# Optimization experiments

Hardware: AMD Instinct MI355X
Metric: run time of the kernel (lower is better)

Reference implementation:

```python
import jax, jax.numpy as jnp
import numpy as np

B, S, D = 2, 2048, 2048
H, KVH, HD = 16, 4, 128
ROT = 64  # partial rotary dims (cos/sin last dim = ROT//2)
WINDOW = 1024
EPS = 1e-6


def _rmsnorm(x, scale=None):
    x32 = x.astype(jnp.float32)
    y = x32 * jax.lax.rsqrt(jnp.mean(x32 * x32, axis=-1, keepdims=True) + EPS)
    if scale is not None:
        y = y * (1.0 + scale.astype(jnp.float32))
    return y.astype(x.dtype)


def _rope(x, cos, sin):
    # x: [b, h, s, hd]; rotate first ROT dims, pass through the rest
    x_rot, x_pass = x[..., :ROT], x[..., ROT:]
    x1, x2 = x_rot[..., :ROT // 2], x_rot[..., ROT // 2:]
    rotated = jnp.concatenate([-x2, x1], axis=-1)
    cos_f = jnp.concatenate([cos, cos], axis=-1)[None, None].astype(x.dtype)
    sin_f = jnp.concatenate([sin, sin], axis=-1)[None, None].astype(x.dtype)
    return jnp.concatenate([x_rot * cos_f + rotated * sin_f, x_pass], axis=-1)


def setup_inputs() -> dict:
    key = jax.random.key(0)
    ks = jax.random.split(key, 6)
    x = jax.random.normal(ks[0], (B, S, D), jnp.float32)
    # causal + sliding-window mask (True = masked out)
    i = jnp.arange(S)
    rel = i[:, None] - i[None, :]  # query - key
    mask = (rel < 0) | (rel >= WINDOW)
    # RoPE tables
    inv_freq = 1.0 / (10000.0 ** (jnp.arange(0, ROT, 2, dtype=jnp.float32) / ROT))
    t = jnp.arange(S, dtype=jnp.float32)[:, None] * inv_freq[None, :]  # [S, ROT//2]
    cos, sin = jnp.cos(t), jnp.sin(t)
    init = 0.02
    Wq = jax.random.normal(ks[1], (D, H * HD), jnp.float32) * init
    Wk = jax.random.normal(ks[2], (D, KVH * HD), jnp.float32) * init
    Wv = jax.random.normal(ks[3], (D, KVH * HD), jnp.float32) * init
    Wo = jax.random.normal(ks[4], (H * HD, D), jnp.float32) * init
    q_scale = jnp.zeros((HD,), jnp.float32)  # Gemma RMSNorm weight init = 0, applied as (1+w)
    k_scale = jnp.zeros((HD,), jnp.float32)
    return {"x": x, "mask": mask, "cos": cos, "sin": sin,
            "Wq": Wq, "Wk": Wk, "Wv": Wv, "Wo": Wo,
            "q_scale": q_scale, "k_scale": k_scale}


def reference(x, mask, cos, sin, Wq, Wk, Wv, Wo, q_scale, k_scale):
    b, s, _ = x.shape
    G = H // KVH  # group size
    q = (x @ Wq).reshape(b, s, H, HD).transpose(0, 2, 1, 3)      # [b,H,s,hd]
    q = _rope(_rmsnorm(q, q_scale), cos, sin)
    k = (x @ Wk).reshape(b, s, KVH, HD).transpose(0, 2, 1, 3)    # [b,KVH,s,hd]
    k = _rope(_rmsnorm(k, k_scale), cos, sin)
    v = _rmsnorm((x @ Wv).reshape(b, s, KVH, HD).transpose(0, 2, 1, 3))
    # grouped-head attention (equivalent to repeat_interleave of k/v over groups)
    qg = q.reshape(b, KVH, G, s, HD)
    scores = jnp.einsum('bkgqd,bkld->bkgql', qg, k)              # no 1/sqrt(hd): QK-norm model
    scores = jnp.where(mask[None, None, None], -jnp.inf, scores)
    w = jax.nn.softmax(scores.astype(jnp.float32), axis=-1).astype(q.dtype)
    ctx = jnp.einsum('bkgql,bkld->bkgqd', w, v)                  # [b,KVH,G,s,hd]
    ctx = ctx.reshape(b, H, s, HD).transpose(0, 2, 1, 3).reshape(b, s, H * HD)
    return ctx @ Wo
```

## Files before the change

kernel.cpp:

```cpp
#include <hip/hip_runtime.h>
#include <stdint.h>

#define B_ 2
#define S_ 2048
#define D_ 2048
#define H_ 16
#define KVH_ 4
#define HD_ 128
#define ROT_ 64
#define WINDOW_ 1024
#define EPS_ 1e-6f
#define M_ (B_ * S_)
#define NQKV_ 3072

#define QBLK 128
#define KVBLK 64

typedef unsigned short ushort_t;
typedef _Float16 f16;
typedef float f32x4 __attribute__((ext_vector_type(4)));
typedef f16 f16x8 __attribute__((ext_vector_type(8)));

#define NINF (-__builtin_inff())

__device__ __forceinline__ void gload16(const void* g, void* l) {
  __builtin_amdgcn_global_load_lds(
      (const __attribute__((address_space(1))) void*)g,
      (__attribute__((address_space(3))) void*)l, 16, 0, 0);
}

__launch_bounds__(256, 4)
__global__ void cast_f32_f16(const float* __restrict__ src, f16* __restrict__ dst, int n8) {
  int i = blockIdx.x * 256 + threadIdx.x;
  if (i >= n8) return;
  float4 a = reinterpret_cast<const float4*>(src)[i * 2];
  float4 b = reinterpret_cast<const float4*>(src)[i * 2 + 1];
  f16x8 o = { (f16)a.x, (f16)a.y, (f16)a.z, (f16)a.w,
              (f16)b.x, (f16)b.y, (f16)b.z, (f16)b.w };
  reinterpret_cast<f16x8*>(dst)[i] = o;
}

__launch_bounds__(256, 4)
__global__ void transpose_f32_f16(const float* __restrict__ src, f16* __restrict__ dst,
                                  int R, int C) {
  __shared__ float tile[32][33];
  int c0 = blockIdx.x * 32, r0 = blockIdx.y * 32;
  int tx = threadIdx.x & 31, ty = threadIdx.x >> 5;
#pragma unroll
  for (int i = 0; i < 32; i += 8)
    tile[ty + i][tx] = src[(size_t)(r0 + ty + i) * C + c0 + tx];
  __syncthreads();
#pragma unroll
  for (int i = 0; i < 32; i += 8)
    dst[(size_t)(c0 + ty + i) * R + r0 + tx] = (f16)tile[tx][ty + i];
}

__launch_bounds__(256, 4)
__global__ void transpose16(const ushort_t* __restrict__ src, ushort_t* __restrict__ dst,
                            int R, int C) {
  __shared__ ushort_t tile[32][33];
  size_t base = (size_t)blockIdx.z * R * C;
  src += base; dst += base;
  int c0 = blockIdx.x * 32, r0 = blockIdx.y * 32;
  int tx = threadIdx.x & 31, ty = threadIdx.x >> 5;
#pragma unroll
  for (int i = 0; i < 32; i += 8)
    tile[ty + i][tx] = src[(size_t)(r0 + ty + i) * C + c0 + tx];
  __syncthreads();
#pragma unroll
  for (int i = 0; i < 32; i += 8)
    dst[(size_t)(c0 + ty + i) * R + r0 + tx] = tile[tx][ty + i];
}

__launch_bounds__(256, 2)
__global__ void gemm_f16(const f16* __restrict__ A, const f16* __restrict__ Bt,
                         float* __restrict__ C, int M, int N, int K) {
  __shared__ __attribute__((aligned(16))) f16 As[128][64];
  __shared__ __attribute__((aligned(16))) f16 Bs[128][64];
  const int gx = gridDim.x;
  const int nwg = gx * gridDim.y;
  const int flat = blockIdx.y * gx + blockIdx.x;
  const int q8 = nwg >> 3;
  const int id2 = (flat & 7) * q8 + (flat >> 3);
  const int bm = (id2 / gx) * 128, bn = (id2 % gx) * 128;
  const int tid = threadIdx.x;
  const int lane = tid & 63, wid = tid >> 6;
  const int wm = (wid >> 1) * 64, wn = (wid & 1) * 64;
  const int rr = lane & 15, rg = lane >> 4;
  const int sw = (((lane & 7) ^ (lane >> 3)) << 4);
  const int srw = lane >> 3;
  const char* Ab = (const char*)A + ((size_t)(bm + wid * 32 + srw) * K) * 2 + sw;
  const char* Bb = (const char*)Bt + ((size_t)(bn + wid * 32 + srw) * K) * 2 + sw;
  f32x4 acc[4][4] = {};
  for (int k0 = 0; k0 < K; k0 += 64) {
    __syncthreads();
#pragma unroll
    for (int g = 0; g < 4; ++g) {
      gload16(Ab + (size_t)(g * 8) * K * 2 + (size_t)k0 * 2,
              (char*)&As[0][0] + (wid * 32 + g * 8) * 128);
      gload16(Bb + (size_t)(g * 8) * K * 2 + (size_t)k0 * 2,
              (char*)&Bs[0][0] + (wid * 32 + g * 8) * 128);
    }
    __syncthreads();
    f16x8 af[4][2], bf[4][2];
#pragma unroll
    for (int i = 0; i < 4; ++i)
#pragma unroll
      for (int kk = 0; kk < 2; ++kk) {
        af[i][kk] = *reinterpret_cast<const f16x8*>(
            (const char*)&As[0][0] + (wm + i * 16 + rr) * 128 +
            ((kk * 64 + rg * 16) ^ ((rr & 7) << 4)));
        bf[i][kk] = *reinterpret_cast<const f16x8*>(
            (const char*)&Bs[0][0] + (wn + i * 16 + rr) * 128 +
            ((kk * 64 + rg * 16) ^ ((rr & 7) << 4)));
      }
#pragma unroll
    for (int kk = 0; kk < 2; ++kk)
#pragma unroll
      for (int i = 0; i < 4; ++i)
#pragma unroll
        for (int j = 0; j < 4; ++j)
          acc[i][j] = __builtin_amdgcn_mfma_f32_16x16x32_f16(af[i][kk], bf[j][kk],
                                                             acc[i][j], 0, 0, 0);
  }
#pragma unroll
  for (int i = 0; i < 4; ++i)
#pragma unroll
    for (int j = 0; j < 4; ++j)
#pragma unroll
      for (int r = 0; r < 4; ++r)
        C[(size_t)(bm + wm + i * 16 + rg * 4 + r) * N + (bn + wn + j * 16 + rr)] = acc[i][j][r];
}

__launch_bounds__(256, 4)
__global__ void norm_rope_kv(const float* __restrict__ qkv, const float* __restrict__ cosb,
                             const float* __restrict__ sinb, const float* __restrict__ ksc,
                             f16* __restrict__ kf, f16* __restrict__ vb) {
  int gw = blockIdx.x * 4 + (threadIdx.x >> 6);
  int lane = threadIdx.x & 63;
  int row = gw >> 3, c = gw & 7;
  int b = row >> 11, s = row & (S_ - 1);
  int col = (c < 4) ? (2048 + c * 128) : (2560 + (c - 4) * 128);
  const float* src = qkv + (size_t)row * NQKV_ + col;
  float2 v = *reinterpret_cast<const float2*>(src + lane * 2);
  float ss = v.x * v.x + v.y * v.y;
#pragma unroll
  for (int off = 32; off; off >>= 1) ss += __shfl_xor(ss, off);
  float inv = rsqrtf(ss * (1.0f / HD_) + EPS_);
  float x0 = v.x * inv, x1 = v.y * inv;
  int d0 = lane * 2;
  f16* dst;
  size_t idx;
  if (c < 4) {
    x0 *= (1.0f + ksc[d0]);
    x1 *= (1.0f + ksc[d0 + 1]);
    float y0 = __shfl_xor(x0, 16);
    float y1 = __shfl_xor(x1, 16);
    if (d0 < ROT_) {
      int dm = d0 & 31;
      float cs0 = cosb[s * 32 + dm],     sn0 = sinb[s * 32 + dm];
      float cs1 = cosb[s * 32 + dm + 1], sn1 = sinb[s * 32 + dm + 1];
      if (d0 < 32) { x0 = x0 * cs0 - y0 * sn0; x1 = x1 * cs1 - y1 * sn1; }
      else         { x0 = x0 * cs0 + y0 * sn0; x1 = x1 * cs1 + y1 * sn1; }
    }
    dst = kf; idx = ((size_t)((b * KVH_ + c) * S_ + s)) * HD_ + d0;
  } else {
    dst = vb; idx = ((size_t)((b * KVH_ + (c - 4)) * S_ + s)) * HD_ + d0;
  }
  f16 o[2] = { (f16)x0, (f16)x1 };
  unsigned int pk; __builtin_memcpy(&pk, o, 4);
  *reinterpret_cast<unsigned int*>(dst + idx) = pk;
}

__launch_bounds__(512, 4)
__global__ void flash_attn(const float* __restrict__ qkv, const float* __restrict__ cosb,
                           const float* __restrict__ sinb, const float* __restrict__ qsc,
                           const f16* __restrict__ kfp, const f16* __restrict__ vt,
                           f16* __restrict__ ctxf) {
  __shared__ __attribute__((aligned(16))) f16 Ks[2][KVBLK][128];
  __shared__ __attribute__((aligned(16))) f16 Vs[2][128][KVBLK];
  __shared__ __attribute__((aligned(16))) f16 Pb[8][16][40];
  const int id = blockIdx.x;
  const int g8 = id & 7, wvb = id >> 3;
  const int b = g8 >> 2, kvh = g8 & 3;
  const int h = kvh * 4 + (wvb >> 4);
  const int qtile = wvb & 15;
  const int tid = threadIdx.x;
  const int lane = tid & 63, w = tid >> 6;
  const int rr = lane & 15, rg = lane >> 4;
  const int qBase = qtile * QBLK;
  const int qw = qBase + w * 16;
  const f16* Kh = kfp + (size_t)(b * KVH_ + kvh) * S_ * HD_;
  const f16* Vh = vt  + (size_t)(b * KVH_ + kvh) * HD_ * S_;

  f16x8 qf[4];
  {
    const int srow = qw + rr;
    const float* qrow = qkv + (size_t)(b * S_ + srow) * NQKV_ + h * HD_;
    float qv[4][8];
    float ssq = 0.f;
#pragma unroll
    for (int kk = 0; kk < 4; ++kk) {
      float4 u0 = *reinterpret_cast<const float4*>(qrow + kk * 32 + rg * 8);
      float4 u1 = *reinterpret_cast<const float4*>(qrow + kk * 32 + rg * 8 + 4);
      qv[kk][0] = u0.x; qv[kk][1] = u0.y; qv[kk][2] = u0.z; qv[kk][3] = u0.w;
      qv[kk][4] = u1.x; qv[kk][5] = u1.y; qv[kk][6] = u1.z; qv[kk][7] = u1.w;
#pragma unroll
      for (int j = 0; j < 8; ++j) ssq += qv[kk][j] * qv[kk][j];
    }
    ssq += __shfl_xor(ssq, 16);
    ssq += __shfl_xor(ssq, 32);
    float inv = rsqrtf(ssq * (1.0f / HD_) + EPS_);
#pragma unroll
    for (int kk = 0; kk < 4; ++kk)
#pragma unroll
      for (int j = 0; j < 8; ++j)
        qv[kk][j] *= inv * (1.0f + qsc[kk * 32 + rg * 8 + j]);
    const float* cs = cosb + (size_t)srow * 32;
    const float* sn = sinb + (size_t)srow * 32;
#pragma unroll
    for (int j = 0; j < 8; ++j) {
      int d = rg * 8 + j;
      float c = cs[d], s = sn[d];
      float x0 = qv[0][j], x1 = qv[1][j];
      qv[0][j] = x0 * c - x1 * s;
      qv[1][j] = x1 * c + x0 * s;
    }
#pragma unroll
    for (int kk = 0; kk < 4; ++kk)
#pragma unroll
      for (int j = 0; j < 8; ++j)
        qf[kk][j] = (f16)qv[kk][j];
  }

  f32x4 acc[8] = {};
  f32x4 accl = {};
  float m_run[4];
#pragma unroll
  for (int r = 0; r < 4; ++r) m_run[r] = NINF;
  const f16x8 ones = { (f16)1, (f16)1, (f16)1, (f16)1, (f16)1, (f16)1, (f16)1, (f16)1 };

  int kvStart = qBase - (WINDOW_ - 1);
  if (kvStart < 0) kvStart = 0;
  kvStart &= ~(KVBLK - 1);
  const int ntile = (qBase + QBLK - kvStart) / KVBLK;

  const int k_r0 = lane >> 4;
  const int k_cb = (lane & 15) * 16;
  const int v_r0 = lane >> 3;
  const int v_cb = (lane & 7) * 16;

#define STAGE(bufs, key0_)                                                           \
  do {                                                                               \
    _Pragma("unroll")                                                                \
    for (int gg = 0; gg < 2; ++gg) {                                                 \
      int krow = gg * 4 + k_r0;                                                      \
      gload16((const char*)Kh + (size_t)((key0_) + w * 8 + krow) * 256 +             \
                  (k_cb ^ ((krow & 7) << 4)),                                        \
              (char*)&Ks[bufs][0][0] + (w * 8 + gg * 4) * 256);                      \
      int vrow = gg * 8 + v_r0;                                                      \
      gload16((const char*)Vh + (size_t)(w * 16 + vrow) * (S_ * 2) +                 \
                  (size_t)(key0_) * 2 + (v_cb ^ ((vrow & 7) << 4)),                  \
              (char*)&Vs[bufs][0][0] + (w * 16 + gg * 8) * 128);                     \
    }                                                                                \
  } while (0)

  STAGE(0, kvStart);
  __syncthreads();

  for (int t = 0; t < ntile; ++t) {
    const int key0 = kvStart + t * KVBLK;
    const int buf = t & 1;
    if (t + 1 < ntile) STAGE(buf ^ 1, key0 + KVBLK);

    f32x4 sc[4];
#pragma unroll
    for (int nt = 0; nt < 4; ++nt) {
      const int rt = nt * 16 + rr;
      const char* kbase = (const char*)&Ks[buf][0][0] + rt * 256;
      const int swz = (rt & 7) << 4;
      f32x4 s = {};
#pragma unroll
      for (int kk = 0; kk < 4; ++kk) {
        f16x8 kfr = *reinterpret_cast<const f16x8*>(kbase + ((kk * 64 + rg * 16) ^ swz));
        s = __builtin_amdgcn_mfma_f32_16x16x32_f16(qf[kk], kfr, s, 0, 0, 0);
      }
      sc[nt] = s;
    }

    const bool interior = (key0 + 63 <= qw) && (key0 >= qw - 1008);
    if (!interior) {
#pragma unroll
      for (int nt = 0; nt < 4; ++nt)
#pragma unroll
        for (int r = 0; r < 4; ++r) {
          int qi = qw + rg * 4 + r;
          int kj = key0 + nt * 16 + rr;
          bool valid = (kj <= qi) && (qi - kj < WINDOW_);
          if (!valid) sc[nt][r] = NINF;
        }
    }

    float tmax[4];
#pragma unroll
    for (int r = 0; r < 4; ++r)
      tmax[r] = fmaxf(fmaxf(sc[0][r], sc[1][r]), fmaxf(sc[2][r], sc[3][r]));
#pragma unroll
    for (int off = 1; off < 16; off <<= 1)
#pragma unroll
      for (int r = 0; r < 4; ++r)
        tmax[r] = fmaxf(tmax[r], __shfl_xor(tmax[r], off));

    float alpha[4], msafe[4];
#pragma unroll
    for (int r = 0; r < 4; ++r) {
      float mn = fmaxf(m_run[r], tmax[r]);
      msafe[r] = (mn == NINF) ? 0.f : mn;
      alpha[r] = (m_run[r] == NINF) ? 0.f : __expf(m_run[r] - mn);
      m_run[r] = mn;
    }
#pragma unroll
    for (int nt = 0; nt < 4; ++nt)
#pragma unroll
      for (int r = 0; r < 4; ++r)
        sc[nt][r] = __expf(sc[nt][r] - msafe[r]);
#pragma unroll
    for (int n = 0; n < 8; ++n)
#pragma unroll
      for (int r = 0; r < 4; ++r) acc[n][r] *= alpha[r];
#pragma unroll
    for (int r = 0; r < 4; ++r) accl[r] *= alpha[r];

#pragma unroll
    for (int nt = 0; nt < 2; ++nt)
#pragma unroll
      for (int r = 0; r < 4; ++r)
        Pb[w][rg * 4 + r][nt * 16 + rr] = (f16)sc[nt][r];
    f16x8 pf0 = *reinterpret_cast<const f16x8*>(&Pb[w][rr][rg * 8]);
#pragma unroll
    for (int nt = 0; nt < 2; ++nt)
#pragma unroll
      for (int r = 0; r < 4; ++r)
        Pb[w][rg * 4 + r][nt * 16 + rr] = (f16)sc[2 + nt][r];
    f16x8 pf1 = *reinterpret_cast<const f16x8*>(&Pb[w][rr][rg * 8]);

    __builtin_amdgcn_s_setprio(1);
#pragma unroll
    for (int n = 0; n < 8; ++n) {
      const int d = n * 16 + rr;
      const char* vbase = (const char*)&Vs[buf][0][0] + d * 128;
      const int swz = (d & 7) << 4;
      f16x8 vf0 = *reinterpret_cast<const f16x8*>(vbase + ((rg * 16) ^ swz));
      f16x8 vf1 = *reinterpret_cast<const f16x8*>(vbase + ((64 + rg * 16) ^ swz));
      acc[n] = __builtin_amdgcn_mfma_f32_16x16x32_f16(pf0, vf0, acc[n], 0, 0, 0);
      acc[n] = __builtin_amdgcn_mfma_f32_16x16x32_f16(pf1, vf1, acc[n], 0, 0, 0);
    }
    accl = __builtin_amdgcn_mfma_f32_16x16x32_f16(pf0, ones, accl, 0, 0, 0);
    accl = __builtin_amdgcn_mfma_f32_16x16x32_f16(pf1, ones, accl, 0, 0, 0);
    __builtin_amdgcn_s_setprio(0);

    __syncthreads();
  }
#undef STAGE

#pragma unroll
  for (int n = 0; n < 8; ++n)
#pragma unroll
    for (int r = 0; r < 4; ++r) {
      float o = acc[n][r] / accl[r];
      int qi = qw + rg * 4 + r;
      ctxf[(size_t)(b * S_ + qi) * D_ + h * HD_ + n * 16 + rr] = (f16)o;
    }
}

extern "C" void kernel_launch(void* const* d_in, const int* in_sizes, int n_in,
                              void* d_out, int out_size, void* d_ws, size_t ws_size,
                              hipStream_t stream) {
  const float* x    = (const float*)d_in[0];
  const float* cosb = (const float*)d_in[2];
  const float* sinb = (const float*)d_in[3];
  const float* Wq   = (const float*)d_in[4];
  const float* Wk   = (const float*)d_in[5];
  const float* Wv   = (const float*)d_in[6];
  const float* Wo   = (const float*)d_in[7];
  const float* qsc  = (const float*)d_in[8];
  const float* ksc  = (const float*)d_in[9];
  float* out = (float*)d_out;

  char* ws = (char*)d_ws;
  const size_t MB = 1ull << 20;
  f16* xh    = (f16*)(ws + 0 * MB);
  f16* ctxf  = (f16*)(ws + 0 * MB);
  f16* wqkvT = (f16*)(ws + 16 * MB);
  f16* kf    = (f16*)(ws + 16 * MB);
  f16* vb    = (f16*)(ws + 20 * MB);
  f16* vtb   = (f16*)(ws + 24 * MB);
  f16* woT   = (f16*)(ws + 28 * MB);
  float* qkv = (float*)(ws + 36 * MB);

  cast_f32_f16<<<dim3(M_ * D_ / 8 / 256), 256, 0, stream>>>(x, xh, M_ * D_ / 8);
  transpose_f32_f16<<<dim3(64, 64), 256, 0, stream>>>(Wq, wqkvT, D_, 2048);
  transpose_f32_f16<<<dim3(16, 64), 256, 0, stream>>>(Wk, wqkvT + (size_t)2048 * D_, D_, 512);
  transpose_f32_f16<<<dim3(16, 64), 256, 0, stream>>>(Wv, wqkvT + (size_t)2560 * D_, D_, 512);
  transpose_f32_f16<<<dim3(64, 64), 256, 0, stream>>>(Wo, woT, D_, D_);
  gemm_f16<<<dim3(NQKV_ / 128, M_ / 128), 256, 0, stream>>>(xh, wqkvT, qkv, M_, NQKV_, D_);
  norm_rope_kv<<<dim3(M_ * 8 / 4), 256, 0, stream>>>(qkv, cosb, sinb, ksc, kf, vb);
  transpose16<<<dim3(HD_ / 32, S_ / 32, B_ * KVH_), 256, 0, stream>>>(
      (const ushort_t*)vb, (ushort_t*)vtb, S_, HD_);
  flash_attn<<<dim3((S_ / QBLK) * H_ * B_), 512, 0, stream>>>(
      qkv, cosb, sinb, qsc, kf, vtb, ctxf);
  gemm_f16<<<dim3(D_ / 128, M_ / 128), 256, 0, stream>>>(ctxf, woT, out, M_, D_, D_);
}
```

Before: 219.5 us.

## Drop LDS K/V staging, use per-wave tiles, exp2 softmax with deferred rescale

The flash attention kernel no longer stages K/V tiles through LDS with a double buffer and barriers. Each wave now reads K and V fragments straight from global memory. Blocks shrink to 4 waves, each owning a 16-row query strip chosen so the strips are strided and the causal work is balanced. Separately, LOG2E is folded into K so softmax can use exp2, and the rescale of the accumulator is skipped unless the running max grows by more than a threshold. The trade-off is that the same K/V data is re-read from global or L2 by every wave with no LDS reuse, in exchange for fewer barriers and more blocks.

```diff
diff --git a/kernel.cpp b/kernel.cpp
--- a/kernel.cpp
+++ b/kernel.cpp
@@ -13,8 +13,9 @@
 #define M_ (B_ * S_)
 #define NQKV_ 3072
 
-#define QBLK 128
 #define KVBLK 64
+#define LOG2E 1.44269504088896340736f
+#define DEFER_THR 8.0f
 
 typedef unsigned short ushort_t;
 typedef _Float16 f16;
@@ -22,6 +23,7 @@
 typedef f16 f16x8 __attribute__((ext_vector_type(8)));
 
 #define NINF (-__builtin_inff())
+#define EXP2F(x) __builtin_exp2f(x)
 
 __device__ __forceinline__ void gload16(const void* g, void* l) {
   __builtin_amdgcn_global_load_lds(
@@ -163,6 +165,7 @@
       if (d0 < 32) { x0 = x0 * cs0 - y0 * sn0; x1 = x1 * cs1 - y1 * sn1; }
       else         { x0 = x0 * cs0 + y0 * sn0; x1 = x1 * cs1 + y1 * sn1; }
     }
+    x0 *= LOG2E; x1 *= LOG2E;
     dst = kf; idx = ((size_t)((b * KVH_ + c) * S_ + s)) * HD_ + d0;
   } else {
     dst = vb; idx = ((size_t)((b * KVH_ + (c - 4)) * S_ + s)) * HD_ + d0;
@@ -172,26 +175,22 @@
   *reinterpret_cast<unsigned int*>(dst + idx) = pk;
 }
 
-__launch_bounds__(512, 4)
+__launch_bounds__(256, 4)
 __global__ void flash_attn(const float* __restrict__ qkv, const float* __restrict__ cosb,
                            const float* __restrict__ sinb, const float* __restrict__ qsc,
                            const f16* __restrict__ kfp, const f16* __restrict__ vt,
                            f16* __restrict__ ctxf) {
-  __shared__ __attribute__((aligned(16))) f16 Ks[2][KVBLK][128];
-  __shared__ __attribute__((aligned(16))) f16 Vs[2][128][KVBLK];
-  __shared__ __attribute__((aligned(16))) f16 Pb[8][16][40];
+  __shared__ __attribute__((aligned(16))) f16 Pb[4][16][40];
   const int id = blockIdx.x;
-  const int g8 = id & 7, wvb = id >> 3;
+  const int g8 = id & 7, rest = id >> 3;
   const int b = g8 >> 2, kvh = g8 & 3;
-  const int h = kvh * 4 + (wvb >> 4);
-  const int qtile = wvb & 15;
-  const int tid = threadIdx.x;
-  const int lane = tid & 63, w = tid >> 6;
+  const int hh = rest >> 5, j = rest & 31;
+  const int h = kvh * 4 + hh;
+  const int lane = threadIdx.x & 63, w = threadIdx.x >> 6;
   const int rr = lane & 15, rg = lane >> 4;
-  const int qBase = qtile * QBLK;
-  const int qw = qBase + w * 16;
-  const f16* Kh = kfp + (size_t)(b * KVH_ + kvh) * S_ * HD_;
-  const f16* Vh = vt  + (size_t)(b * KVH_ + kvh) * HD_ * S_;
+  const int qw = (j + 32 * w) * 16;
+  const char* Kh = (const char*)(kfp + (size_t)(b * KVH_ + kvh) * S_ * HD_);
+  const char* Vh = (const char*)(vt  + (size_t)(b * KVH_ + kvh) * HD_ * S_);
 
   f16x8 qf[4];
   {
@@ -206,7 +205,7 @@
       qv[kk][0] = u0.x; qv[kk][1] = u0.y; qv[kk][2] = u0.z; qv[kk][3] = u0.w;
       qv[kk][4] = u1.x; qv[kk][5] = u1.y; qv[kk][6] = u1.z; qv[kk][7] = u1.w;
 #pragma unroll
-      for (int j = 0; j < 8; ++j) ssq += qv[kk][j] * qv[kk][j];
+      for (int j2 = 0; j2 < 8; ++j2) ssq += qv[kk][j2] * qv[kk][j2];
     }
     ssq += __shfl_xor(ssq, 16);
     ssq += __shfl_xor(ssq, 32);
@@ -214,75 +213,51 @@
 #pragma unroll
     for (int kk = 0; kk < 4; ++kk)
 #pragma unroll
-      for (int j = 0; j < 8; ++j)
-        qv[kk][j] *= inv * (1.0f + qsc[kk * 32 + rg * 8 + j]);
+      for (int j2 = 0; j2 < 8; ++j2)
+        qv[kk][j2] *= inv * (1.0f + qsc[kk * 32 + rg * 8 + j2]);
     const float* cs = cosb + (size_t)srow * 32;
     const float* sn = sinb + (size_t)srow * 32;
 #pragma unroll
-    for (int j = 0; j < 8; ++j) {
-      int d = rg * 8 + j;
+    for (int j2 = 0; j2 < 8; ++j2) {
+      int d = rg * 8 + j2;
       float c = cs[d], s = sn[d];
-      float x0 = qv[0][j], x1 = qv[1][j];
-      qv[0][j] = x0 * c - x1 * s;
-      qv[1][j] = x1 * c + x0 * s;
+      float x0 = qv[0][j2], x1 = qv[1][j2];
+      qv[0][j2] = x0 * c - x1 * s;
+      qv[1][j2] = x1 * c + x0 * s;
     }
 #pragma unroll
     for (int kk = 0; kk < 4; ++kk)
 #pragma unroll
-      for (int j = 0; j < 8; ++j)
-        qf[kk][j] = (f16)qv[kk][j];
+      for (int j2 = 0; j2 < 8; ++j2)
+        qf[kk][j2] = (f16)qv[kk][j2];
   }
 
   f32x4 acc[8] = {};
   f32x4 accl = {};
-  float m_run[4];
-#pragma unroll
-  for (int r = 0; r < 4; ++r) m_run[r] = NINF;
+  float m_run[4], msafe[4];
+#pragma unroll
+  for (int r = 0; r < 4; ++r) { m_run[r] = NINF; msafe[r] = 0.f; }
   const f16x8 ones = { (f16)1, (f16)1, (f16)1, (f16)1, (f16)1, (f16)1, (f16)1, (f16)1 };
 
-  int kvStart = qBase - (WINDOW_ - 1);
+  int kvStart = qw - (WINDOW_ - 1);
   if (kvStart < 0) kvStart = 0;
   kvStart &= ~(KVBLK - 1);
-  const int ntile = (qBase + QBLK - kvStart) / KVBLK;
-
-  const int k_r0 = lane >> 4;
-  const int k_cb = (lane & 15) * 16;
-  const int v_r0 = lane >> 3;
-  const int v_cb = (lane & 7) * 16;
-
-#define STAGE(bufs, key0_)                                                           \
-  do {                                                                               \
-    _Pragma("unroll")                                                                \
-    for (int gg = 0; gg < 2; ++gg) {                                                 \
-      int krow = gg * 4 + k_r0;                                                      \
-      gload16((const char*)Kh + (size_t)((key0_) + w * 8 + krow) * 256 +             \
-                  (k_cb ^ ((krow & 7) << 4)),                                        \
-              (char*)&Ks[bufs][0][0] + (w * 8 + gg * 4) * 256);                      \
-      int vrow = gg * 8 + v_r0;                                                      \
-      gload16((const char*)Vh + (size_t)(w * 16 + vrow) * (S_ * 2) +                 \
-                  (size_t)(key0_) * 2 + (v_cb ^ ((vrow & 7) << 4)),                  \
-              (char*)&Vs[bufs][0][0] + (w * 16 + gg * 8) * 128);                     \
-    }                                                                                \
-  } while (0)
-
-  STAGE(0, kvStart);
-  __syncthreads();
+  const int ntile = ((qw + 16 - kvStart) + KVBLK - 1) >> 6;
+
+  const char* kl = Kh + (size_t)rr * 256 + rg * 16;
+  const char* vl = Vh + (size_t)rr * (S_ * 2) + rg * 16;
 
   for (int t = 0; t < ntile; ++t) {
     const int key0 = kvStart + t * KVBLK;
-    const int buf = t & 1;
-    if (t + 1 < ntile) STAGE(buf ^ 1, key0 + KVBLK);
 
     f32x4 sc[4];
 #pragma unroll
     for (int nt = 0; nt < 4; ++nt) {
-      const int rt = nt * 16 + rr;
-      const char* kbase = (const char*)&Ks[buf][0][0] + rt * 256;
-      const int swz = (rt & 7) << 4;
+      const char* kb = kl + (size_t)(key0 + nt * 16) * 256;
       f32x4 s = {};
 #pragma unroll
       for (int kk = 0; kk < 4; ++kk) {
-        f16x8 kfr = *reinterpret_cast<const f16x8*>(kbase + ((kk * 64 + rg * 16) ^ swz));
+        f16x8 kfr = *reinterpret_cast<const f16x8*>(kb + kk * 64);
         s = __builtin_amdgcn_mfma_f32_16x16x32_f16(qf[kk], kfr, s, 0, 0, 0);
       }
       sc[nt] = s;
@@ -311,25 +286,31 @@
       for (int r = 0; r < 4; ++r)
         tmax[r] = fmaxf(tmax[r], __shfl_xor(tmax[r], off));
 
-    float alpha[4], msafe[4];
-#pragma unroll
-    for (int r = 0; r < 4; ++r) {
-      float mn = fmaxf(m_run[r], tmax[r]);
-      msafe[r] = (mn == NINF) ? 0.f : mn;
-      alpha[r] = (m_run[r] == NINF) ? 0.f : __expf(m_run[r] - mn);
-      m_run[r] = mn;
+    bool defer = true;
+#pragma unroll
+    for (int r = 0; r < 4; ++r)
+      defer = defer && (tmax[r] - m_run[r] <= DEFER_THR);
+    if (!__all(defer)) {
+      float alpha[4];
+#pragma unroll
+      for (int r = 0; r < 4; ++r) {
+        float mn = fmaxf(m_run[r], tmax[r]);
+        alpha[r] = (m_run[r] == NINF) ? 0.f : EXP2F(m_run[r] - mn);
+        m_run[r] = mn;
+        msafe[r] = (mn == NINF) ? 0.f : mn;
+      }
+#pragma unroll
+      for (int n = 0; n < 8; ++n)
+#pragma unroll
+        for (int r = 0; r < 4; ++r) acc[n][r] *= alpha[r];
+#pragma unroll
+      for (int r = 0; r < 4; ++r) accl[r] *= alpha[r];
     }
 #pragma unroll
     for (int nt = 0; nt < 4; ++nt)
 #pragma unroll
       for (int r = 0; r < 4; ++r)
-        sc[nt][r] = __expf(sc[nt][r] - msafe[r]);
-#pragma unroll
-    for (int n = 0; n < 8; ++n)
-#pragma unroll
-      for (int r = 0; r < 4; ++r) acc[n][r] *= alpha[r];
-#pragma unroll
-    for (int r = 0; r < 4; ++r) accl[r] *= alpha[r];
+        sc[nt][r] = EXP2F(sc[nt][r] - msafe[r]);
 
 #pragma unroll
     for (int nt = 0; nt < 2; ++nt)
@@ -347,21 +328,16 @@
     __builtin_amdgcn_s_setprio(1);
 #pragma unroll
     for (int n = 0; n < 8; ++n) {
-      const int d = n * 16 + rr;
-      const char* vbase = (const char*)&Vs[buf][0][0] + d * 128;
-      const int swz = (d & 7) << 4;
-      f16x8 vf0 = *reinterpret_cast<const f16x8*>(vbase + ((rg * 16) ^ swz));
-      f16x8 vf1 = *reinterpret_cast<const f16x8*>(vbase + ((64 + rg * 16) ^ swz));
+      const char* vb2 = vl + (size_t)n * 16 * (S_ * 2) + (size_t)key0 * 2;
+      f16x8 vf0 = *reinterpret_cast<const f16x8*>(vb2);
+      f16x8 vf1 = *reinterpret_cast<const f16x8*>(vb2 + 64);
       acc[n] = __builtin_amdgcn_mfma_f32_16x16x32_f16(pf0, vf0, acc[n], 0, 0, 0);
       acc[n] = __builtin_amdgcn_mfma_f32_16x16x32_f16(pf1, vf1, acc[n], 0, 0, 0);
     }
     accl = __builtin_amdgcn_mfma_f32_16x16x32_f16(pf0, ones, accl, 0, 0, 0);
     accl = __builtin_amdgcn_mfma_f32_16x16x32_f16(pf1, ones, accl, 0, 0, 0);
     __builtin_amdgcn_s_setprio(0);
-
-    __syncthreads();
   }
-#undef STAGE
 
 #pragma unroll
   for (int n = 0; n < 8; ++n)
@@ -407,7 +383,7 @@
   norm_rope_kv<<<dim3(M_ * 8 / 4), 256, 0, stream>>>(qkv, cosb, sinb, ksc, kf, vb);
   transpose16<<<dim3(HD_ / 32, S_ / 32, B_ * KVH_), 256, 0, stream>>>(
       (const ushort_t*)vb, (ushort_t*)vtb, S_, HD_);
-  flash_attn<<<dim3((S_ / QBLK) * H_ * B_), 512, 0, stream>>>(
+  flash_attn<<<dim3((S_ / 64) * H_ * B_), 256, 0, stream>>>(
       qkv, cosb, sinb, qsc, kf, vtb, ctxf);
   gemm_f16<<<dim3(D_ / 128, M_ / 128), 256, 0, stream>>>(ctxf, woT, out, M_, D_, D_);
 }
```

New measurement: 358.2 us. 1.63x slower.

## Restructure flash attention to 4 waves with 32 query rows each and lazy rescale

Applied to the files above, without the earlier changes.

The flash attention kernel now runs 256 threads per block, and each wave handles two 16-row query sub-blocks, so every K fragment read from LDS feeds two MFMAs. Several changes ride along: log2(e) is folded into K so softmax can use exp2, rescaling of the accumulators is skipped while the running max grows by no more than a threshold, KV tiles entirely outside a wave's window are skipped, and blocks are reordered so long-running query tiles launch first. The costs are more registers per wave and fewer waves per block, and the deferred rescale depends on the threshold keeping exponents in range.

```diff
diff --git a/kernel.cpp b/kernel.cpp
--- a/kernel.cpp
+++ b/kernel.cpp
@@ -15,6 +15,8 @@
 
 #define QBLK 128
 #define KVBLK 64
+#define LOG2E 1.44269504088896340736f
+#define DEFER_THR 8.0f
 
 typedef unsigned short ushort_t;
 typedef _Float16 f16;
@@ -22,6 +24,7 @@
 typedef f16 f16x8 __attribute__((ext_vector_type(8)));
 
 #define NINF (-__builtin_inff())
+#define EXP2F(x) __builtin_exp2f(x)
 
 __device__ __forceinline__ void gload16(const void* g, void* l) {
   __builtin_amdgcn_global_load_lds(
@@ -163,6 +166,7 @@
       if (d0 < 32) { x0 = x0 * cs0 - y0 * sn0; x1 = x1 * cs1 - y1 * sn1; }
       else         { x0 = x0 * cs0 + y0 * sn0; x1 = x1 * cs1 + y1 * sn1; }
     }
+    x0 *= LOG2E; x1 *= LOG2E;
     dst = kf; idx = ((size_t)((b * KVH_ + c) * S_ + s)) * HD_ + d0;
   } else {
     dst = vb; idx = ((size_t)((b * KVH_ + (c - 4)) * S_ + s)) * HD_ + d0;
@@ -172,30 +176,32 @@
   *reinterpret_cast<unsigned int*>(dst + idx) = pk;
 }
 
-__launch_bounds__(512, 4)
+__launch_bounds__(256, 2)
 __global__ void flash_attn(const float* __restrict__ qkv, const float* __restrict__ cosb,
                            const float* __restrict__ sinb, const float* __restrict__ qsc,
                            const f16* __restrict__ kfp, const f16* __restrict__ vt,
                            f16* __restrict__ ctxf) {
   __shared__ __attribute__((aligned(16))) f16 Ks[2][KVBLK][128];
   __shared__ __attribute__((aligned(16))) f16 Vs[2][128][KVBLK];
-  __shared__ __attribute__((aligned(16))) f16 Pb[8][16][40];
+  __shared__ __attribute__((aligned(16))) f16 Pb[4][32][40];
   const int id = blockIdx.x;
-  const int g8 = id & 7, wvb = id >> 3;
+  const int g8 = id & 7, rest = id >> 3;
   const int b = g8 >> 2, kvh = g8 & 3;
-  const int h = kvh * 4 + (wvb >> 4);
-  const int qtile = wvb & 15;
-  const int tid = threadIdx.x;
-  const int lane = tid & 63, w = tid >> 6;
+  int hh, qtile;
+  if (rest < 32) { hh = rest >> 3; qtile = 8 + (rest & 7); }
+  else { int lv = rest - 32; hh = lv >> 3; qtile = lv & 7; }
+  const int h = kvh * 4 + hh;
+  const int lane = threadIdx.x & 63, w = threadIdx.x >> 6;
   const int rr = lane & 15, rg = lane >> 4;
   const int qBase = qtile * QBLK;
-  const int qw = qBase + w * 16;
+  const int qw = qBase + w * 32;
   const f16* Kh = kfp + (size_t)(b * KVH_ + kvh) * S_ * HD_;
   const f16* Vh = vt  + (size_t)(b * KVH_ + kvh) * HD_ * S_;
 
-  f16x8 qf[4];
-  {
-    const int srow = qw + rr;
+  f16x8 qf[2][4];
+#pragma unroll
+  for (int rb = 0; rb < 2; ++rb) {
+    const int srow = qw + rb * 16 + rr;
     const float* qrow = qkv + (size_t)(b * S_ + srow) * NQKV_ + h * HD_;
     float qv[4][8];
     float ssq = 0.f;
@@ -230,20 +236,22 @@
     for (int kk = 0; kk < 4; ++kk)
 #pragma unroll
       for (int j = 0; j < 8; ++j)
-        qf[kk][j] = (f16)qv[kk][j];
+        qf[rb][kk][j] = (f16)qv[kk][j];
   }
 
-  f32x4 acc[8] = {};
-  f32x4 accl = {};
-  float m_run[4];
-#pragma unroll
-  for (int r = 0; r < 4; ++r) m_run[r] = NINF;
+  f32x4 acc[2][8] = {};
+  f32x4 accl[2] = {};
+  float m_run[2][4], msafe[2][4];
+#pragma unroll
+  for (int rb = 0; rb < 2; ++rb)
+#pragma unroll
+    for (int r = 0; r < 4; ++r) { m_run[rb][r] = NINF; msafe[rb][r] = 0.f; }
   const f16x8 ones = { (f16)1, (f16)1, (f16)1, (f16)1, (f16)1, (f16)1, (f16)1, (f16)1 };
 
   int kvStart = qBase - (WINDOW_ - 1);
   if (kvStart < 0) kvStart = 0;
   kvStart &= ~(KVBLK - 1);
-  const int ntile = (qBase + QBLK - kvStart) / KVBLK;
+  const int ntile = (qBase + QBLK - kvStart) >> 6;
 
   const int k_r0 = lane >> 4;
   const int k_cb = (lane & 15) * 16;
@@ -253,15 +261,15 @@
 #define STAGE(bufs, key0_)                                                           \
   do {                                                                               \
     _Pragma("unroll")                                                                \
-    for (int gg = 0; gg < 2; ++gg) {                                                 \
+    for (int gg = 0; gg < 4; ++gg) {                                                 \
       int krow = gg * 4 + k_r0;                                                      \
-      gload16((const char*)Kh + (size_t)((key0_) + w * 8 + krow) * 256 +             \
+      gload16((const char*)Kh + (size_t)((key0_) + w * 16 + krow) * 256 +            \
                   (k_cb ^ ((krow & 7) << 4)),                                        \
-              (char*)&Ks[bufs][0][0] + (w * 8 + gg * 4) * 256);                      \
+              (char*)&Ks[bufs][0][0] + (w * 16 + gg * 4) * 256);                     \
       int vrow = gg * 8 + v_r0;                                                      \
-      gload16((const char*)Vh + (size_t)(w * 16 + vrow) * (S_ * 2) +                 \
+      gload16((const char*)Vh + (size_t)(w * 32 + vrow) * (S_ * 2) +                 \
                   (size_t)(key0_) * 2 + (v_cb ^ ((vrow & 7) << 4)),                  \
-              (char*)&Vs[bufs][0][0] + (w * 16 + gg * 8) * 128);                     \
+              (char*)&Vs[bufs][0][0] + (w * 32 + gg * 8) * 128);                     \
     }                                                                                \
   } while (0)
 
@@ -273,104 +281,139 @@
     const int buf = t & 1;
     if (t + 1 < ntile) STAGE(buf ^ 1, key0 + KVBLK);
 
-    f32x4 sc[4];
-#pragma unroll
-    for (int nt = 0; nt < 4; ++nt) {
-      const int rt = nt * 16 + rr;
-      const char* kbase = (const char*)&Ks[buf][0][0] + rt * 256;
-      const int swz = (rt & 7) << 4;
-      f32x4 s = {};
-#pragma unroll
-      for (int kk = 0; kk < 4; ++kk) {
-        f16x8 kfr = *reinterpret_cast<const f16x8*>(kbase + ((kk * 64 + rg * 16) ^ swz));
-        s = __builtin_amdgcn_mfma_f32_16x16x32_f16(qf[kk], kfr, s, 0, 0, 0);
-      }
-      sc[nt] = s;
+    const bool live = (key0 <= qw + 31) && (key0 + 63 >= qw - (WINDOW_ - 1));
+    if (live) {
+      f32x4 sc[2][4];
+#pragma unroll
+      for (int nt = 0; nt < 4; ++nt) {
+        const int rt = nt * 16 + rr;
+        const char* kbase = (const char*)&Ks[buf][0][0] + rt * 256;
+        const int swz = (rt & 7) << 4;
+        f16x8 kfr[4];
+#pragma unroll
+        for (int kk = 0; kk < 4; ++kk)
+          kfr[kk] = *reinterpret_cast<const f16x8*>(kbase + ((kk * 64 + rg * 16) ^ swz));
+        f32x4 s0 = {}, s1 = {};
+#pragma unroll
+        for (int kk = 0; kk < 4; ++kk) {
+          s0 = __builtin_amdgcn_mfma_f32_16x16x32_f16(qf[0][kk], kfr[kk], s0, 0, 0, 0);
+          s1 = __builtin_amdgcn_mfma_f32_16x16x32_f16(qf[1][kk], kfr[kk], s1, 0, 0, 0);
+        }
+        sc[0][nt] = s0; sc[1][nt] = s1;
+      }
+
+      const bool interior = (key0 + 63 <= qw) && (key0 >= qw - 992);
+      if (!interior) {
+#pragma unroll
+        for (int rb = 0; rb < 2; ++rb)
+#pragma unroll
+          for (int nt = 0; nt < 4; ++nt)
+#pragma unroll
+            for (int r = 0; r < 4; ++r) {
+              int qi = qw + rb * 16 + rg * 4 + r;
+              int kj = key0 + nt * 16 + rr;
+              bool valid = (kj <= qi) && (qi - kj < WINDOW_);
+              if (!valid) sc[rb][nt][r] = NINF;
+            }
+      }
+
+      float tmax[2][4];
+#pragma unroll
+      for (int rb = 0; rb < 2; ++rb)
+#pragma unroll
+        for (int r = 0; r < 4; ++r)
+          tmax[rb][r] = fmaxf(fmaxf(sc[rb][0][r], sc[rb][1][r]),
+                              fmaxf(sc[rb][2][r], sc[rb][3][r]));
+#pragma unroll
+      for (int off = 1; off < 16; off <<= 1)
+#pragma unroll
+        for (int rb = 0; rb < 2; ++rb)
+#pragma unroll
+          for (int r = 0; r < 4; ++r)
+            tmax[rb][r] = fmaxf(tmax[rb][r], __shfl_xor(tmax[rb][r], off));
+
+      bool defer = true;
+#pragma unroll
+      for (int rb = 0; rb < 2; ++rb)
+#pragma unroll
+        for (int r = 0; r < 4; ++r)
+          defer = defer && (tmax[rb][r] - m_run[rb][r] <= DEFER_THR);
+      if (!__all(defer)) {
+#pragma unroll
+        for (int rb = 0; rb < 2; ++rb) {
+          float alpha[4];
+#pragma unroll
+          for (int r = 0; r < 4; ++r) {
+            float mn = fmaxf(m_run[rb][r], tmax[rb][r]);
+            alpha[r] = (m_run[rb][r] == NINF) ? 0.f : EXP2F(m_run[rb][r] - mn);
+            m_run[rb][r] = mn;
+            msafe[rb][r] = (mn == NINF) ? 0.f : mn;
+          }
+#pragma unroll
+          for (int n = 0; n < 8; ++n)
+#pragma unroll
+            for (int r = 0; r < 4; ++r) acc[rb][n][r] *= alpha[r];
+#pragma unroll
+          for (int r = 0; r < 4; ++r) accl[rb][r] *= alpha[r];
+        }
+      }
+#pragma unroll
+      for (int rb = 0; rb < 2; ++rb)
+#pragma unroll
+        for (int nt = 0; nt < 4; ++nt)
+#pragma unroll
+          for (int r = 0; r < 4; ++r)
+            sc[rb][nt][r] = EXP2F(sc[rb][nt][r] - msafe[rb][r]);
+
+      f16x8 pf[2][2];
+#pragma unroll
+      for (int p = 0; p < 2; ++p) {
+#pragma unroll
+        for (int rb = 0; rb < 2; ++rb)
+#pragma unroll
+          for (int nt2 = 0; nt2 < 2; ++nt2)
+#pragma unroll
+            for (int r = 0; r < 4; ++r)
+              Pb[w][rb * 16 + rg * 4 + r][nt2 * 16 + rr] = (f16)sc[rb][p * 2 + nt2][r];
+        pf[0][p] = *reinterpret_cast<const f16x8*>(&Pb[w][rr][rg * 8]);
+        pf[1][p] = *reinterpret_cast<const f16x8*>(&Pb[w][16 + rr][rg * 8]);
+      }
+
+      __builtin_amdgcn_s_setprio(1);
+#pragma unroll
+      for (int n = 0; n < 8; ++n) {
+        const int d = n * 16 + rr;
+        const char* vbase = (const char*)&Vs[buf][0][0] + d * 128;
+        const int swz = (d & 7) << 4;
+        f16x8 vf0 = *reinterpret_cast<const f16x8*>(vbase + ((rg * 16) ^ swz));
+        f16x8 vf1 = *reinterpret_cast<const f16x8*>(vbase + ((64 + rg * 16) ^ swz));
+        acc[0][n] = __builtin_amdgcn_mfma_f32_16x16x32_f16(pf[0][0], vf0, acc[0][n], 0, 0, 0);
+        acc[0][n] = __builtin_amdgcn_mfma_f32_16x16x32_f16(pf[0][1], vf1, acc[0][n], 0, 0, 0);
+        acc[1][n] = __builtin_amdgcn_mfma_f32_16x16x32_f16(pf[1][0], vf0, acc[1][n], 0, 0, 0);
+        acc[1][n] = __builtin_amdgcn_mfma_f32_16x16x32_f16(pf[1][1], vf1, acc[1][n], 0, 0, 0);
+      }
+#pragma unroll
+      for (int rb = 0; rb < 2; ++rb) {
+        accl[rb] = __builtin_amdgcn_mfma_f32_16x16x32_f16(pf[rb][0], ones, accl[rb], 0, 0, 0);
+        accl[rb] = __builtin_amdgcn_mfma_f32_16x16x32_f16(pf[rb][1], ones, accl[rb], 0, 0, 0);
+      }
+      __builtin_amdgcn_s_setprio(0);
     }
-
-    const bool interior = (key0 + 63 <= qw) && (key0 >= qw - 1008);
-    if (!interior) {
-#pragma unroll
-      for (int nt = 0; nt < 4; ++nt)
-#pragma unroll
-        for (int r = 0; r < 4; ++r) {
-          int qi = qw + rg * 4 + r;
-          int kj = key0 + nt * 16 + rr;
-          bool valid = (kj <= qi) && (qi - kj < WINDOW_);
-          if (!valid) sc[nt][r] = NINF;
-        }
-    }
-
-    float tmax[4];
-#pragma unroll
-    for (int r = 0; r < 4; ++r)
-      tmax[r] = fmaxf(fmaxf(sc[0][r], sc[1][r]), fmaxf(sc[2][r], sc[3][r]));
-#pragma unroll
-    for (int off = 1; off < 16; off <<= 1)
-#pragma unroll
-      for (int r = 0; r < 4; ++r)
-        tmax[r] = fmaxf(tmax[r], __shfl_xor(tmax[r], off));
-
-    float alpha[4], msafe[4];
-#pragma unroll
-    for (int r = 0; r < 4; ++r) {
-      float mn = fmaxf(m_run[r], tmax[r]);
-      msafe[r] = (mn == NINF) ? 0.f : mn;
-      alpha[r] = (m_run[r] == NINF) ? 0.f : __expf(m_run[r] - mn);
-      m_run[r] = mn;
-    }
-#pragma unroll
-    for (int nt = 0; nt < 4; ++nt)
-#pragma unroll
-      for (int r = 0; r < 4; ++r)
-        sc[nt][r] = __expf(sc[nt][r] - msafe[r]);
-#pragma unroll
-    for (int n = 0; n < 8; ++n)
-#pragma unroll
-      for (int r = 0; r < 4; ++r) acc[n][r] *= alpha[r];
-#pragma unroll
-    for (int r = 0; r < 4; ++r) accl[r] *= alpha[r];
-
-#pragma unroll
-    for (int nt = 0; nt < 2; ++nt)
-#pragma unroll
-      for (int r = 0; r < 4; ++r)
-        Pb[w][rg * 4 + r][nt * 16 + rr] = (f16)sc[nt][r];
-    f16x8 pf0 = *reinterpret_cast<const f16x8*>(&Pb[w][rr][rg * 8]);
-#pragma unroll
-    for (int nt = 0; nt < 2; ++nt)
-#pragma unroll
-      for (int r = 0; r < 4; ++r)
-        Pb[w][rg * 4 + r][nt * 16 + rr] = (f16)sc[2 + nt][r];
-    f16x8 pf1 = *reinterpret_cast<const f16x8*>(&Pb[w][rr][rg * 8]);
-
-    __builtin_amdgcn_s_setprio(1);
-#pragma unroll
-    for (int n = 0; n < 8; ++n) {
-      const int d = n * 16 + rr;
-      const char* vbase = (const char*)&Vs[buf][0][0] + d * 128;
-      const int swz = (d & 7) << 4;
-      f16x8 vf0 = *reinterpret_cast<const f16x8*>(vbase + ((rg * 16) ^ swz));
-      f16x8 vf1 = *reinterpret_cast<const f16x8*>(vbase + ((64 + rg * 16) ^ swz));
-      acc[n] = __builtin_amdgcn_mfma_f32_16x16x32_f16(pf0, vf0, acc[n], 0, 0, 0);
-      acc[n] = __builtin_amdgcn_mfma_f32_16x16x32_f16(pf1, vf1, acc[n], 0, 0, 0);
-    }
-    accl = __builtin_amdgcn_mfma_f32_16x16x32_f16(pf0, ones, accl, 0, 0, 0);
-    accl = __builtin_amdgcn_mfma_f32_16x16x32_f16(pf1, ones, accl, 0, 0, 0);
-    __builtin_amdgcn_s_setprio(0);
 
     __syncthreads();
   }
 #undef STAGE
 
 #pragma unroll
-  for (int n = 0; n < 8; ++n)
-#pragma unroll
-    for (int r = 0; r < 4; ++r) {
-      float o = acc[n][r] / accl[r];
-      int qi = qw + rg * 4 + r;
-      ctxf[(size_t)(b * S_ + qi) * D_ + h * HD_ + n * 16 + rr] = (f16)o;
-    }
+  for (int rb = 0; rb < 2; ++rb)
+#pragma unroll
+    for (int n = 0; n < 8; ++n)
+#pragma unroll
+      for (int r = 0; r < 4; ++r) {
+        float o = acc[rb][n][r] / accl[rb][r];
+        int qi = qw + rb * 16 + rg * 4 + r;
+        ctxf[(size_t)(b * S_ + qi) * D_ + h * HD_ + n * 16 + rr] = (f16)o;
+      }
 }
 
 extern "C" void kernel_launch(void* const* d_in, const int* in_sizes, int n_in,
@@ -407,7 +450,7 @@
   norm_rope_kv<<<dim3(M_ * 8 / 4), 256, 0, stream>>>(qkv, cosb, sinb, ksc, kf, vb);
   transpose16<<<dim3(HD_ / 32, S_ / 32, B_ * KVH_), 256, 0, stream>>>(
       (const ushort_t*)vb, (ushort_t*)vtb, S_, HD_);
-  flash_attn<<<dim3((S_ / QBLK) * H_ * B_), 512, 0, stream>>>(
+  flash_attn<<<dim3((S_ / QBLK) * H_ * B_), 256, 0, stream>>>(
       qkv, cosb, sinb, qsc, kf, vtb, ctxf);
   gemm_f16<<<dim3(D_ / 128, M_ / 128), 256, 0, stream>>>(ctxf, woT, out, M_, D_, D_);
 }
```

Measured after the change: 222.7 us. No clear change (+1.4%).
